# Kernel tuning notes

Measured on AMD Instinct MI355X. Metric: run time of the kernel, lower is better.

## Reference

```python
import jax, jax.numpy as jnp
import numpy as np
import math

DIM = 512
HEADS = 8
DH = DIM // HEADS
B, C, H, W = 2, 512, 48, 48


def setup_inputs() -> dict:
    key = jax.random.key(0)
    k1, k2, k3, k4 = jax.random.split(key, 4)
    x = jax.random.normal(k1, (B, C, H, W), dtype=jnp.float32)
    # torch Linear weights: [out_features, in_features]
    w_qkv = jax.random.normal(k2, (3 * DIM, DIM), dtype=jnp.float32) * (DIM ** -0.5)
    w_out = jax.random.normal(k3, (DIM, DIM), dtype=jnp.float32) * (DIM ** -0.5)
    b_out = jax.random.normal(k4, (DIM,), dtype=jnp.float32) * 0.01
    wavelength = jnp.asarray(0.1, dtype=jnp.float32)
    return {"x": x, "w_qkv": w_qkv, "w_out": w_out, "b_out": b_out, "wavelength": wavelength}


def reference(x, w_qkv, w_out, b_out, wavelength):
    b, c, h, w = x.shape
    n = h * w
    scale = DH ** -0.5

    x_flat = x.reshape(b, c, n).transpose(0, 2, 1)  # [B, N, C]
    qkv = jnp.einsum('bnc,dc->bnd', x_flat, w_qkv)   # [B, N, 3*DIM]
    q, k, v = jnp.split(qkv, 3, axis=-1)

    def to_heads(t):
        return t.reshape(b, n, HEADS, DH).transpose(0, 2, 1, 3)  # [B, h, N, dh]

    q, k, v = to_heads(q), to_heads(k), to_heads(v)

    dots = jnp.einsum('bhid,bhjd->bhij', q, k) * scale  # [B, h, N, N]

    # Fresnel interference bias over spatial positions
    yy, xx = jnp.meshgrid(jnp.arange(h), jnp.arange(w), indexing='ij')
    positions = jnp.stack([yy, xx], axis=-1).astype(jnp.float32).reshape(-1, 2)  # [N, 2]
    pos_diff = positions[None, :, :] - positions[:, None, :]  # [N, N, 2]
    distances = jnp.sqrt(jnp.sum(pos_diff ** 2, axis=-1) + 1e-8)  # [N, N]
    phase = 2.0 * math.pi * distances / (jnp.abs(wavelength) * h + 1e-6)
    interference = jnp.cos(phase)

    dots = dots + interference[None, None, :, :] * 0.1
    attn = jax.nn.softmax(dots, axis=-1)
    out = jnp.einsum('bhij,bhjd->bhid', attn, v)  # [B, h, N, dh]
    out = out.transpose(0, 2, 1, 3).reshape(b, n, HEADS * DH)  # [B, N, DIM]
    out = jnp.einsum('bnd,od->bno', out, w_out) + b_out
    return out.transpose(0, 2, 1).reshape(b, c, h, w)
```

## Files before the change

### kernel.cpp

```cpp
#include <hip/hip_runtime.h>
#include <math.h>

#define BB 2
#define CC 512
#define NN 2304
#define NH 8
#define DD 512
#define D3 1536
#define WIDTH 48
#define C1 0.18033688f

typedef _Float16 h8 __attribute__((ext_vector_type(8)));
typedef _Float16 h4 __attribute__((ext_vector_type(4)));
typedef _Float16 h2 __attribute__((ext_vector_type(2)));
typedef float f4 __attribute__((ext_vector_type(4)));

__device__ __forceinline__ void gload16(const void* g, void* s) {
  __builtin_amdgcn_global_load_lds(
      (const __attribute__((address_space(1))) unsigned int*)g,
      (__attribute__((address_space(3))) unsigned int*)s, 16, 0, 0);
}

__global__ __launch_bounds__(128) void btf_k(const float* __restrict__ wavp,
                                             _Float16* __restrict__ btf)
{
  const int t = threadIdx.x;
  const int qbk = blockIdx.x, ktk = blockIdx.y;
  const int w = t >> 6, quad = (t >> 4) & 3, l15 = t & 15;
  const float pc = 6.283185307179586f / (fabsf(wavp[0]) * (float)WIDTH + 1e-6f);
  _Float16* o = btf + (((size_t)qbk * 36 + ktk) * 128 + t) * 32;
#pragma unroll
  for (int g = 0; g < 4; ++g) {
    h8 v;
#pragma unroll
    for (int e = 0; e < 8; ++e) {
      const int j = g * 8 + e;
      const int nt = j >> 4, mt = (j >> 2) & 3, r = j & 3;
      const int q = qbk * 64 + w * 32 + nt * 16 + l15;
      const int k = ktk * 64 + mt * 16 + quad * 4 + r;
      const float dy = (float)(q / WIDTH) - (float)(k / WIDTH);
      const float dx = (float)(q % WIDTH) - (float)(k % WIDTH);
      const float dist = sqrtf(dy * dy + dx * dx + 1e-8f);
      v[e] = (_Float16)(0.1f * __cosf(dist * pc) * 1.44269504f);
    }
    *(h8*)(o + g * 8) = v;
  }
}

__global__ __launch_bounds__(256) void tx_k(const float* __restrict__ x,
                                            _Float16* __restrict__ xt)
{
  __shared__ float Ls[32][33];
  const int t = threadIdx.x;
  const int n0 = blockIdx.x * 32, c0 = blockIdx.y * 32, b = blockIdx.z;
#pragma unroll
  for (int p = 0; p < 4; ++p) {
    const int cl = (t >> 5) + p * 8, nl = t & 31;
    Ls[cl][nl] = x[((size_t)b * CC + c0 + cl) * NN + n0 + nl];
  }
  __syncthreads();
#pragma unroll
  for (int p = 0; p < 2; ++p) {
    const int nl = (t >> 4) + p * 16, cl = (t & 15) * 2;
    h2 v = {(_Float16)Ls[cl][nl], (_Float16)Ls[cl + 1][nl]};
    *(h2*)(xt + ((size_t)b * NN + n0 + nl) * CC + c0 + cl) = v;
  }
}

__global__ __launch_bounds__(256) void convw_k(const float* __restrict__ wq,
                                               const float* __restrict__ wo,
                                               _Float16* __restrict__ wqh,
                                               _Float16* __restrict__ woh)
{
  const int idx = blockIdx.x * 256 + threadIdx.x;
  const int NQ = (D3 * CC) / 4;
  if (idx < NQ) {
    float4 v = *(const float4*)(wq + (size_t)idx * 4);
    h4 o = {(_Float16)v.x, (_Float16)v.y, (_Float16)v.z, (_Float16)v.w};
    *(h4*)(wqh + (size_t)idx * 4) = o;
  } else {
    const int j = idx - NQ;
    float4 v = *(const float4*)(wo + (size_t)j * 4);
    h4 o = {(_Float16)v.x, (_Float16)v.y, (_Float16)v.z, (_Float16)v.w};
    *(h4*)(woh + (size_t)j * 4) = o;
  }
}

__global__ __launch_bounds__(256) void qkv_gemm_k(
    const _Float16* __restrict__ xt, const _Float16* __restrict__ wqh,
    _Float16* __restrict__ qb, _Float16* __restrict__ kb,
    _Float16* __restrict__ vb)
{
  __shared__ _Float16 Xs[128][32];
  __shared__ _Float16 Ws[128][32];
  const int t = threadIdx.x;
  const int lane = t & 63, w = t >> 6;
  const int l15 = lane & 15, quad = lane >> 4;
  const int wm = w & 1, wn = w >> 1;
  const int n0 = blockIdx.x * 128;
  const int d0 = blockIdx.y * 128;
  const int b  = blockIdx.z;
  const bool isv = (d0 >= 2 * DD);
  const _Float16* xb = xt + (size_t)b * NN * CC;

  const int srow = lane >> 2, scol = (lane & 3) * 8;

  f4 acc[4][4];
#pragma unroll
  for (int mt = 0; mt < 4; ++mt)
#pragma unroll
    for (int nt = 0; nt < 4; ++nt) acc[mt][nt] = (f4)(0.f);

  for (int c0 = 0; c0 < CC; c0 += 32) {
#pragma unroll
    for (int r = 0; r < 2; ++r) {
      const int ci = w + r * 4;
      const int row = ci * 16 + srow;
      gload16(xb + (size_t)(n0 + row) * CC + c0 + scol, &Xs[0][0] + ci * 512);
      gload16(wqh + (size_t)(d0 + row) * CC + c0 + scol, &Ws[0][0] + ci * 512);
    }
    __syncthreads();

    h8 wfr[4], xfr[4];
#pragma unroll
    for (int mt = 0; mt < 4; ++mt)
      wfr[mt] = *(const h8*)&Ws[wm * 64 + mt * 16 + l15][quad * 8];
#pragma unroll
    for (int nt = 0; nt < 4; ++nt)
      xfr[nt] = *(const h8*)&Xs[wn * 64 + nt * 16 + l15][quad * 8];

    if (!isv) {
#pragma unroll
      for (int mt = 0; mt < 4; ++mt)
#pragma unroll
        for (int nt = 0; nt < 4; ++nt)
          acc[mt][nt] = __builtin_amdgcn_mfma_f32_16x16x32_f16(
              wfr[mt], xfr[nt], acc[mt][nt], 0, 0, 0);
    } else {
#pragma unroll
      for (int mt = 0; mt < 4; ++mt)
#pragma unroll
        for (int nt = 0; nt < 4; ++nt)
          acc[mt][nt] = __builtin_amdgcn_mfma_f32_16x16x32_f16(
              xfr[nt], wfr[mt], acc[mt][nt], 0, 0, 0);
    }
    __syncthreads();
  }

  if (!isv) {
    const int which = d0 >> 9;
    _Float16* buf = which == 0 ? qb : kb;
    const int h = ((d0 & 511) >> 6) + wm;
#pragma unroll
    for (int mt = 0; mt < 4; ++mt) {
      const int dh = mt * 16 + quad * 4;
#pragma unroll
      for (int nt = 0; nt < 4; ++nt) {
        const int token = n0 + wn * 64 + nt * 16 + l15;
        h4 o = {(_Float16)acc[mt][nt][0], (_Float16)acc[mt][nt][1],
                (_Float16)acc[mt][nt][2], (_Float16)acc[mt][nt][3]};
        *(h4*)(buf + (((size_t)b * NH + h) * NN + token) * 64 + dh) = o;
      }
    }
  } else {
    const int h = ((d0 - 2 * DD) >> 6) + wm;
#pragma unroll
    for (int mt = 0; mt < 4; ++mt) {
      const int dh = mt * 16 + l15;
#pragma unroll
      for (int nt = 0; nt < 4; ++nt) {
        const int token = n0 + wn * 64 + nt * 16 + quad * 4;
        h4 o = {(_Float16)acc[mt][nt][0], (_Float16)acc[mt][nt][1],
                (_Float16)acc[mt][nt][2], (_Float16)acc[mt][nt][3]};
        *(h4*)(vb + (((size_t)b * NH + h) * 64 + dh) * NN + token) = o;
      }
    }
  }
}

__global__ __launch_bounds__(128, 3) void attn_k(
    const _Float16* __restrict__ qb, const _Float16* __restrict__ kb,
    const _Float16* __restrict__ vb, const _Float16* __restrict__ btf,
    _Float16* __restrict__ op, float* __restrict__ lp)
{
  __shared__ _Float16 Ks[64][72];
  __shared__ _Float16 Vs[64][72];
  __shared__ _Float16 Ps[64][72];

  const int t    = threadIdx.x;
  const int lane = t & 63;
  const int w    = t >> 6;
  const int l15  = lane & 15;
  const int quad = lane >> 4;
  const int qtile = blockIdx.x >> 1;
  const int khalf = blockIdx.x & 1;
  const int n0 = qtile * 64;
  const int h  = blockIdx.y;
  const int b  = blockIdx.z;
  const size_t base = ((size_t)b * NH + h) * NN * 64;
  const _Float16* qp = qb + base;
  const _Float16* kp = kb + base;
  const _Float16* vp = vb + base;

  h8 qf[2][2];
#pragma unroll
  for (int nt = 0; nt < 2; ++nt)
#pragma unroll
    for (int ks = 0; ks < 2; ++ks)
      qf[nt][ks] = *(const h8*)(qp + (size_t)(n0 + w * 32 + nt * 16 + l15) * 64 +
                                ks * 32 + quad * 8);

  f4 oc[4][2];
#pragma unroll
  for (int mt = 0; mt < 4; ++mt)
#pragma unroll
    for (int nt = 0; nt < 2; ++nt) oc[mt][nt] = (f4)(0.f);
  float lacc[2][4] = {};

  const _Float16* bp = btf + (((size_t)qtile * 36 + khalf * 18) * 128 + t) * 32;

  for (int kt = 0; kt < 18; ++kt) {
    const int k0 = (khalf * 18 + kt) * 64;
    h8 kr[4], vr[4], bfr[4];
#pragma unroll
    for (int r = 0; r < 4; ++r) {
      const int c = t + r * 128;
      const int row = c >> 3, off = (c & 7) * 8;
      kr[r] = *(const h8*)(kp + (size_t)(k0 + row) * 64 + off);
      vr[r] = *(const h8*)(vp + (size_t)row * NN + k0 + off);
      bfr[r] = *(const h8*)(bp + r * 8);
    }
    bp += 128 * 32;
    __syncthreads();
#pragma unroll
    for (int r = 0; r < 4; ++r) {
      const int c = t + r * 128;
      const int row = c >> 3, off = (c & 7) * 8;
      *(h8*)&Ks[row][off] = kr[r];
      *(h8*)&Vs[row][off] = vr[r];
    }
    __syncthreads();

    f4 st[4][2];
#pragma unroll
    for (int mt = 0; mt < 4; ++mt)
#pragma unroll
      for (int nt = 0; nt < 2; ++nt) st[mt][nt] = (f4)(0.f);
#pragma unroll
    for (int ks = 0; ks < 2; ++ks) {
#pragma unroll
      for (int mt = 0; mt < 4; ++mt) {
        h8 kf = *(const h8*)&Ks[mt * 16 + l15][ks * 32 + quad * 8];
#pragma unroll
        for (int nt = 0; nt < 2; ++nt)
          st[mt][nt] = __builtin_amdgcn_mfma_f32_16x16x32_f16(
              kf, qf[nt][ks], st[mt][nt], 0, 0, 0);
      }
    }

#pragma unroll
    for (int nt = 0; nt < 2; ++nt) {
      const int q = w * 32 + nt * 16 + l15;
#pragma unroll
      for (int mt = 0; mt < 4; ++mt) {
        h4 pk;
#pragma unroll
        for (int r = 0; r < 4; ++r) {
          const int j = nt * 16 + mt * 4 + r;
          const float bias = (float)bfr[j >> 3][j & 7];
          const float p = __builtin_exp2f(st[mt][nt][r] * C1 + bias);
          lacc[nt][r] += p;
          pk[r] = (_Float16)p;
        }
        *(h4*)&Ps[q][mt * 16 + quad * 4] = pk;
      }
    }

#pragma unroll
    for (int ks = 0; ks < 2; ++ks) {
      h8 pf[2];
#pragma unroll
      for (int nt = 0; nt < 2; ++nt)
        pf[nt] = *(const h8*)&Ps[w * 32 + nt * 16 + l15][ks * 32 + quad * 8];
#pragma unroll
      for (int mt = 0; mt < 4; ++mt) {
        h8 vf = *(const h8*)&Vs[mt * 16 + l15][ks * 32 + quad * 8];
#pragma unroll
        for (int nt = 0; nt < 2; ++nt)
          oc[mt][nt] = __builtin_amdgcn_mfma_f32_16x16x32_f16(
              vf, pf[nt], oc[mt][nt], 0, 0, 0);
      }
    }
  }

#pragma unroll
  for (int nt = 0; nt < 2; ++nt) {
    float l = lacc[nt][0] + lacc[nt][1] + lacc[nt][2] + lacc[nt][3];
    l += __shfl_xor(l, 16);
    l += __shfl_xor(l, 32);
    const float inv = 1.f / l;
    const int qi = n0 + w * 32 + nt * 16 + l15;
    _Float16* od = op + (size_t)khalf * BB * NN * DD +
                   ((size_t)b * NN + qi) * DD + h * 64;
#pragma unroll
    for (int mt = 0; mt < 4; ++mt) {
      const int dh = mt * 16 + quad * 4;
      h4 o = {(_Float16)(oc[mt][nt][0] * inv), (_Float16)(oc[mt][nt][1] * inv),
              (_Float16)(oc[mt][nt][2] * inv), (_Float16)(oc[mt][nt][3] * inv)};
      *(h4*)(od + dh) = o;
    }
    if (quad == 0)
      lp[(size_t)khalf * BB * NH * NN + ((size_t)b * NH + h) * NN + qi] = l;
  }
}

__global__ __launch_bounds__(256) void comb_k(
    const _Float16* __restrict__ op, const float* __restrict__ lp,
    _Float16* __restrict__ ho)
{
  const int idx = blockIdx.x * 256 + threadIdx.x;
  const int d8 = idx & 63;
  const int bn = idx >> 6;
  const int n = bn % NN, b = bn / NN;
  const int h = d8 >> 3;
  const float l0 = lp[((size_t)b * NH + h) * NN + n];
  const float l1 = lp[(size_t)BB * NH * NN + ((size_t)b * NH + h) * NN + n];
  const float inv = 1.f / (l0 + l1);
  const float w0 = l0 * inv, w1 = l1 * inv;
  h8 o0 = *(const h8*)(op + (size_t)bn * DD + d8 * 8);
  h8 o1 = *(const h8*)(op + (size_t)BB * NN * DD + (size_t)bn * DD + d8 * 8);
  h8 r;
#pragma unroll
  for (int i = 0; i < 8; ++i)
    r[i] = (_Float16)((float)o0[i] * w0 + (float)o1[i] * w1);
  *(h8*)(ho + (size_t)bn * DD + d8 * 8) = r;
}

__global__ __launch_bounds__(64) void out_gemm_k(
    const _Float16* __restrict__ ho, const _Float16* __restrict__ woh,
    const float* __restrict__ bias, float* __restrict__ out)
{
  __shared__ _Float16 Hs[64][32];
  __shared__ _Float16 Ws2[64][32];
  const int t = threadIdx.x;
  const int l15 = t & 15, quad = t >> 4;
  const int n0 = blockIdx.x * 64;
  const int o0 = blockIdx.y * 64;
  const int b  = blockIdx.z;
  const int srow = t >> 2, scol = (t & 3) * 8;

  f4 acc[4][4];
#pragma unroll
  for (int mt = 0; mt < 4; ++mt)
#pragma unroll
    for (int nt = 0; nt < 4; ++nt) acc[mt][nt] = (f4)(0.f);

  for (int c0 = 0; c0 < DD; c0 += 32) {
#pragma unroll
    for (int ci = 0; ci < 4; ++ci) {
      const int row = ci * 16 + srow;
      gload16(ho + ((size_t)b * NN + n0 + row) * DD + c0 + scol,
              &Hs[0][0] + ci * 512);
      gload16(woh + (size_t)(o0 + row) * DD + c0 + scol,
              &Ws2[0][0] + ci * 512);
    }
    __syncthreads();
    h8 hf[4], wf[4];
#pragma unroll
    for (int mt = 0; mt < 4; ++mt)
      hf[mt] = *(const h8*)&Hs[mt * 16 + l15][quad * 8];
#pragma unroll
    for (int nt = 0; nt < 4; ++nt)
      wf[nt] = *(const h8*)&Ws2[nt * 16 + l15][quad * 8];
#pragma unroll
    for (int mt = 0; mt < 4; ++mt)
#pragma unroll
      for (int nt = 0; nt < 4; ++nt)
        acc[mt][nt] = __builtin_amdgcn_mfma_f32_16x16x32_f16(
            hf[mt], wf[nt], acc[mt][nt], 0, 0, 0);
    __syncthreads();
  }

#pragma unroll
  for (int nt = 0; nt < 4; ++nt) {
    const int o = o0 + nt * 16 + l15;
    const float bv = bias[o];
#pragma unroll
    for (int mt = 0; mt < 4; ++mt) {
      const int token = n0 + mt * 16 + quad * 4;
      float4 v = {acc[mt][nt][0] + bv, acc[mt][nt][1] + bv,
                  acc[mt][nt][2] + bv, acc[mt][nt][3] + bv};
      *(float4*)(out + ((size_t)b * DD + o) * NN + token) = v;
    }
  }
}

extern "C" void kernel_launch(void* const* d_in, const int* in_sizes, int n_in,
                              void* d_out, int out_size, void* d_ws, size_t ws_size,
                              hipStream_t stream)
{
  (void)in_sizes; (void)n_in; (void)out_size; (void)ws_size;
  const float* x     = (const float*)d_in[0];
  const float* w_qkv = (const float*)d_in[1];
  const float* w_out = (const float*)d_in[2];
  const float* b_out = (const float*)d_in[3];
  const float* wav   = (const float*)d_in[4];
  float* out = (float*)d_out;

  const size_t SZ  = (size_t)BB * NH * NN * 64;
  const size_t BTF = (size_t)36 * 36 * 128 * 32;

  _Float16* qb  = (_Float16*)d_ws;
  _Float16* kb  = qb + SZ;
  _Float16* vb  = kb + SZ;
  _Float16* btf = vb + SZ;
  _Float16* op  = btf + BTF;
  float*    lpf = (float*)(op + 2 * SZ);
  _Float16* woh = (_Float16*)(lpf + 2 * (size_t)BB * NH * NN);
  _Float16* ho  = btf;
  _Float16* xt  = op;
  _Float16* wqh = op + SZ;

  btf_k     <<<dim3(36, 36), 128, 0, stream>>>(wav, btf);
  tx_k      <<<dim3(NN / 32, CC / 32, BB), 256, 0, stream>>>(x, xt);
  convw_k   <<<dim3((D3 * CC + DD * DD) / 1024), 256, 0, stream>>>(w_qkv, w_out, wqh, woh);
  qkv_gemm_k<<<dim3(NN / 128, D3 / 128, BB), 256, 0, stream>>>(xt, wqh, qb, kb, vb);
  attn_k    <<<dim3(NN / 64 * 2, NH, BB), 128, 0, stream>>>(qb, kb, vb, btf, op, lpf);
  comb_k    <<<dim3((BB * NN * 64) / 256), 256, 0, stream>>>(op, lpf, ho);
  out_gemm_k<<<dim3(NN / 64, DD / 64, BB), 64, 0, stream>>>(ho, woh, b_out, out);
}
```

Measured before the change: 168.4 us.

## Compress bias table by tile-difference symmetry, split K three ways, fuse prep kernels

The three preprocessing kernels (bias table, transpose of x, weight conversion) are merged into one launch. The 36x36 bias tile table is shrunk to 213 tiles, indexed by query-key tile offset and query tile mod 3. This works because 64-token tiles shift the 48-wide grid by a periodic pattern. The attention kernel now splits keys three ways instead of two and reuses the K shared-memory buffer for P, which drops the Ps array and raises occupancy to 4 blocks. Packed fp16 conversion is used for P. The combine step merges three partials, which adds an extra sync per tile and more partial-output traffic.

```diff
diff --git a/kernel.cpp b/kernel.cpp
--- a/kernel.cpp
+++ b/kernel.cpp
@@ -10,6 +10,10 @@
 #define WIDTH 48
 #define C1 0.18033688f
 
+#define KSPLIT 3
+#define KTILES 12
+#define NTBL 213
+
 typedef _Float16 h8 __attribute__((ext_vector_type(8)));
 typedef _Float16 h4 __attribute__((ext_vector_type(4)));
 typedef _Float16 h2 __attribute__((ext_vector_type(2)));
@@ -21,68 +25,72 @@
       (__attribute__((address_space(3))) unsigned int*)s, 16, 0, 0);
 }
 
-__global__ __launch_bounds__(128) void btf_k(const float* __restrict__ wavp,
-                                             _Float16* __restrict__ btf)
-{
-  const int t = threadIdx.x;
-  const int qbk = blockIdx.x, ktk = blockIdx.y;
-  const int w = t >> 6, quad = (t >> 4) & 3, l15 = t & 15;
-  const float pc = 6.283185307179586f / (fabsf(wavp[0]) * (float)WIDTH + 1e-6f);
-  _Float16* o = btf + (((size_t)qbk * 36 + ktk) * 128 + t) * 32;
-#pragma unroll
-  for (int g = 0; g < 4; ++g) {
-    h8 v;
-#pragma unroll
-    for (int e = 0; e < 8; ++e) {
-      const int j = g * 8 + e;
-      const int nt = j >> 4, mt = (j >> 2) & 3, r = j & 3;
-      const int q = qbk * 64 + w * 32 + nt * 16 + l15;
-      const int k = ktk * 64 + mt * 16 + quad * 4 + r;
-      const float dy = (float)(q / WIDTH) - (float)(k / WIDTH);
-      const float dx = (float)(q % WIDTH) - (float)(k % WIDTH);
-      const float dist = sqrtf(dy * dy + dx * dx + 1e-8f);
-      v[e] = (_Float16)(0.1f * __cosf(dist * pc) * 1.44269504f);
-    }
-    *(h8*)(o + g * 8) = v;
-  }
-}
-
-__global__ __launch_bounds__(256) void tx_k(const float* __restrict__ x,
-                                            _Float16* __restrict__ xt)
+__global__ __launch_bounds__(256) void prep_k(
+    const float* __restrict__ x, const float* __restrict__ wq,
+    const float* __restrict__ wo, const float* __restrict__ wavp,
+    _Float16* __restrict__ xt, _Float16* __restrict__ wqh,
+    _Float16* __restrict__ woh, _Float16* __restrict__ btf)
 {
   __shared__ float Ls[32][33];
   const int t = threadIdx.x;
-  const int n0 = blockIdx.x * 32, c0 = blockIdx.y * 32, b = blockIdx.z;
-#pragma unroll
-  for (int p = 0; p < 4; ++p) {
-    const int cl = (t >> 5) + p * 8, nl = t & 31;
-    Ls[cl][nl] = x[((size_t)b * CC + c0 + cl) * NN + n0 + nl];
-  }
-  __syncthreads();
-#pragma unroll
-  for (int p = 0; p < 2; ++p) {
-    const int nl = (t >> 4) + p * 16, cl = (t & 15) * 2;
-    h2 v = {(_Float16)Ls[cl][nl], (_Float16)Ls[cl + 1][nl]};
-    *(h2*)(xt + ((size_t)b * NN + n0 + nl) * CC + c0 + cl) = v;
-  }
-}
-
-__global__ __launch_bounds__(256) void convw_k(const float* __restrict__ wq,
-                                               const float* __restrict__ wo,
-                                               _Float16* __restrict__ wqh,
-                                               _Float16* __restrict__ woh)
-{
-  const int idx = blockIdx.x * 256 + threadIdx.x;
-  const int NQ = (D3 * CC) / 4;
-  if (idx < NQ) {
-    float4 v = *(const float4*)(wq + (size_t)idx * 4);
-    h4 o = {(_Float16)v.x, (_Float16)v.y, (_Float16)v.z, (_Float16)v.w};
-    *(h4*)(wqh + (size_t)idx * 4) = o;
+  const int e = blockIdx.x;
+
+  if (e < 2304) {
+    const int n0 = (e % 72) * 32;
+    const int c0 = ((e / 72) % 16) * 32;
+    const int b  = e / 1152;
+#pragma unroll
+    for (int p = 0; p < 4; ++p) {
+      const int cl = (t >> 5) + p * 8, nl = t & 31;
+      Ls[cl][nl] = x[((size_t)b * CC + c0 + cl) * NN + n0 + nl];
+    }
+    __syncthreads();
+#pragma unroll
+    for (int p = 0; p < 2; ++p) {
+      const int nl = (t >> 4) + p * 16, cl = (t & 15) * 2;
+      h2 v = {(_Float16)Ls[cl][nl], (_Float16)Ls[cl + 1][nl]};
+      *(h2*)(xt + ((size_t)b * NN + n0 + nl) * CC + c0 + cl) = v;
+    }
+  } else if (e < 3328) {
+    const int idx = (e - 2304) * 256 + t;
+    const int NQ = (D3 * CC) / 4;
+    if (idx < NQ) {
+      float4 v = *(const float4*)(wq + (size_t)idx * 4);
+      h4 o = {(_Float16)v.x, (_Float16)v.y, (_Float16)v.z, (_Float16)v.w};
+      *(h4*)(wqh + (size_t)idx * 4) = o;
+    } else {
+      const int j = idx - NQ;
+      float4 v = *(const float4*)(wo + (size_t)j * 4);
+      h4 o = {(_Float16)v.x, (_Float16)v.y, (_Float16)v.z, (_Float16)v.w};
+      *(h4*)(woh + (size_t)j * 4) = o;
+    }
   } else {
-    const int j = idx - NQ;
-    float4 v = *(const float4*)(wo + (size_t)j * 4);
-    h4 o = {(_Float16)v.x, (_Float16)v.y, (_Float16)v.z, (_Float16)v.w};
-    *(h4*)(woh + (size_t)j * 4) = o;
+    const int tbl = (e - 3328) * 2 + (t >> 7);
+    if (tbl < NTBL) {
+      const int tid = t & 127;
+      const int dD = tbl / 3, qm = tbl % 3;
+      const int qt0 = qm + 36;
+      const int kt0 = qt0 - (dD - 35);
+      const int w = tid >> 6, quad = (tid >> 4) & 3, l15 = tid & 15;
+      const float pc = 6.283185307179586f / (fabsf(wavp[0]) * (float)WIDTH + 1e-6f);
+      _Float16* o = btf + ((size_t)tbl * 128 + tid) * 32;
+#pragma unroll
+      for (int g = 0; g < 4; ++g) {
+        h8 v;
+#pragma unroll
+        for (int el = 0; el < 8; ++el) {
+          const int j = g * 8 + el;
+          const int nt = j >> 4, mt = (j >> 2) & 3, r = j & 3;
+          const int q = qt0 * 64 + w * 32 + nt * 16 + l15;
+          const int k = kt0 * 64 + mt * 16 + quad * 4 + r;
+          const float dy = (float)(q / WIDTH) - (float)(k / WIDTH);
+          const float dx = (float)(q % WIDTH) - (float)(k % WIDTH);
+          const float dist = sqrtf(dy * dy + dx * dx + 1e-8f);
+          v[el] = (_Float16)(0.1f * __cosf(dist * pc) * 1.44269504f);
+        }
+        *(h8*)(o + g * 8) = v;
+      }
+    }
   }
 }
 
@@ -178,22 +186,21 @@
   }
 }
 
-__global__ __launch_bounds__(128, 3) void attn_k(
+__global__ __launch_bounds__(128, 4) void attn_k(
     const _Float16* __restrict__ qb, const _Float16* __restrict__ kb,
     const _Float16* __restrict__ vb, const _Float16* __restrict__ btf,
     _Float16* __restrict__ op, float* __restrict__ lp)
 {
   __shared__ _Float16 Ks[64][72];
   __shared__ _Float16 Vs[64][72];
-  __shared__ _Float16 Ps[64][72];
 
   const int t    = threadIdx.x;
   const int lane = t & 63;
   const int w    = t >> 6;
   const int l15  = lane & 15;
   const int quad = lane >> 4;
-  const int qtile = blockIdx.x >> 1;
-  const int khalf = blockIdx.x & 1;
+  const int qtile = blockIdx.x / KSPLIT;
+  const int kq    = blockIdx.x % KSPLIT;
   const int n0 = qtile * 64;
   const int h  = blockIdx.y;
   const int b  = blockIdx.z;
@@ -215,12 +222,14 @@
   for (int mt = 0; mt < 4; ++mt)
 #pragma unroll
     for (int nt = 0; nt < 2; ++nt) oc[mt][nt] = (f4)(0.f);
-  float lacc[2][4] = {};
-
-  const _Float16* bp = btf + (((size_t)qtile * 36 + khalf * 18) * 128 + t) * 32;
-
-  for (int kt = 0; kt < 18; ++kt) {
-    const int k0 = (khalf * 18 + kt) * 64;
+  float lac[2][2] = {};
+
+  const int ktg0 = kq * KTILES;
+  const _Float16* bp =
+      btf + ((size_t)((qtile - ktg0 + 35) * 3 + qtile % 3) * 128 + t) * 32;
+
+  for (int kt = 0; kt < KTILES; ++kt) {
+    const int k0 = (ktg0 + kt) * 64;
     h8 kr[4], vr[4], bfr[4];
 #pragma unroll
     for (int r = 0; r < 4; ++r) {
@@ -230,7 +239,7 @@
       vr[r] = *(const h8*)(vp + (size_t)row * NN + k0 + off);
       bfr[r] = *(const h8*)(bp + r * 8);
     }
-    bp += 128 * 32;
+    bp -= 3 * 128 * 32;
     __syncthreads();
 #pragma unroll
     for (int r = 0; r < 4; ++r) {
@@ -258,21 +267,29 @@
       }
     }
 
+    __syncthreads();
+
 #pragma unroll
     for (int nt = 0; nt < 2; ++nt) {
       const int q = w * 32 + nt * 16 + l15;
 #pragma unroll
       for (int mt = 0; mt < 4; ++mt) {
-        h4 pk;
-#pragma unroll
-        for (int r = 0; r < 4; ++r) {
-          const int j = nt * 16 + mt * 4 + r;
-          const float bias = (float)bfr[j >> 3][j & 7];
-          const float p = __builtin_exp2f(st[mt][nt][r] * C1 + bias);
-          lacc[nt][r] += p;
-          pk[r] = (_Float16)p;
-        }
-        *(h4*)&Ps[q][mt * 16 + quad * 4] = pk;
+        const int jb = nt * 16 + mt * 4;
+        const float b0 = (float)bfr[jb >> 3][(jb & 7) + 0];
+        const float b1 = (float)bfr[jb >> 3][(jb & 7) + 1];
+        const float b2 = (float)bfr[jb >> 3][(jb & 7) + 2];
+        const float b3 = (float)bfr[jb >> 3][(jb & 7) + 3];
+        const float p0 = __builtin_exp2f(st[mt][nt][0] * C1 + b0);
+        const float p1 = __builtin_exp2f(st[mt][nt][1] * C1 + b1);
+        const float p2 = __builtin_exp2f(st[mt][nt][2] * C1 + b2);
+        const float p3 = __builtin_exp2f(st[mt][nt][3] * C1 + b3);
+        lac[nt][0] += p0 + p1;
+        lac[nt][1] += p2 + p3;
+        const auto plo = __builtin_amdgcn_cvt_pkrtz(p0, p1);
+        const auto phi = __builtin_amdgcn_cvt_pkrtz(p2, p3);
+        h4 pk = {(_Float16)plo[0], (_Float16)plo[1],
+                 (_Float16)phi[0], (_Float16)phi[1]};
+        *(h4*)&Ks[q][mt * 16 + quad * 4] = pk;
       }
     }
 
@@ -281,7 +298,7 @@
       h8 pf[2];
 #pragma unroll
       for (int nt = 0; nt < 2; ++nt)
-        pf[nt] = *(const h8*)&Ps[w * 32 + nt * 16 + l15][ks * 32 + quad * 8];
+        pf[nt] = *(const h8*)&Ks[w * 32 + nt * 16 + l15][ks * 32 + quad * 8];
 #pragma unroll
       for (int mt = 0; mt < 4; ++mt) {
         h8 vf = *(const h8*)&Vs[mt * 16 + l15][ks * 32 + quad * 8];
@@ -295,12 +312,12 @@
 
 #pragma unroll
   for (int nt = 0; nt < 2; ++nt) {
-    float l = lacc[nt][0] + lacc[nt][1] + lacc[nt][2] + lacc[nt][3];
+    float l = lac[nt][0] + lac[nt][1];
     l += __shfl_xor(l, 16);
     l += __shfl_xor(l, 32);
     const float inv = 1.f / l;
     const int qi = n0 + w * 32 + nt * 16 + l15;
-    _Float16* od = op + (size_t)khalf * BB * NN * DD +
+    _Float16* od = op + (size_t)kq * BB * NN * DD +
                    ((size_t)b * NN + qi) * DD + h * 64;
 #pragma unroll
     for (int mt = 0; mt < 4; ++mt) {
@@ -310,7 +327,7 @@
       *(h4*)(od + dh) = o;
     }
     if (quad == 0)
-      lp[(size_t)khalf * BB * NH * NN + ((size_t)b * NH + h) * NN + qi] = l;
+      lp[(size_t)kq * BB * NH * NN + ((size_t)b * NH + h) * NN + qi] = l;
   }
 }
 
@@ -323,16 +340,21 @@
   const int bn = idx >> 6;
   const int n = bn % NN, b = bn / NN;
   const int h = d8 >> 3;
-  const float l0 = lp[((size_t)b * NH + h) * NN + n];
-  const float l1 = lp[(size_t)BB * NH * NN + ((size_t)b * NH + h) * NN + n];
-  const float inv = 1.f / (l0 + l1);
-  const float w0 = l0 * inv, w1 = l1 * inv;
+  const size_t SL = (size_t)BB * NH * NN;
+  const size_t SO = (size_t)BB * NN * DD;
+  const size_t li = ((size_t)b * NH + h) * NN + n;
+  const float l0 = lp[li];
+  const float l1 = lp[SL + li];
+  const float l2 = lp[2 * SL + li];
+  const float inv = 1.f / (l0 + l1 + l2);
+  const float w0 = l0 * inv, w1 = l1 * inv, w2 = l2 * inv;
   h8 o0 = *(const h8*)(op + (size_t)bn * DD + d8 * 8);
-  h8 o1 = *(const h8*)(op + (size_t)BB * NN * DD + (size_t)bn * DD + d8 * 8);
+  h8 o1 = *(const h8*)(op + SO + (size_t)bn * DD + d8 * 8);
+  h8 o2 = *(const h8*)(op + 2 * SO + (size_t)bn * DD + d8 * 8);
   h8 r;
 #pragma unroll
   for (int i = 0; i < 8; ++i)
-    r[i] = (_Float16)((float)o0[i] * w0 + (float)o1[i] * w1);
+    r[i] = (_Float16)((float)o0[i] * w0 + (float)o1[i] * w1 + (float)o2[i] * w2);
   *(h8*)(ho + (size_t)bn * DD + d8 * 8) = r;
 }
 
@@ -408,24 +430,23 @@
   float* out = (float*)d_out;
 
   const size_t SZ  = (size_t)BB * NH * NN * 64;
-  const size_t BTF = (size_t)36 * 36 * 128 * 32;
+  const size_t BTF = (size_t)NTBL * 128 * 32;
 
   _Float16* qb  = (_Float16*)d_ws;
   _Float16* kb  = qb + SZ;
   _Float16* vb  = kb + SZ;
   _Float16* btf = vb + SZ;
   _Float16* op  = btf + BTF;
-  float*    lpf = (float*)(op + 2 * SZ);
-  _Float16* woh = (_Float16*)(lpf + 2 * (size_t)BB * NH * NN);
-  _Float16* ho  = btf;
+  float*    lpf = (float*)(op + 3 * SZ);
+  _Float16* woh = (_Float16*)(lpf + 3 * (size_t)BB * NH * NN);
+  _Float16* ho  = qb;
   _Float16* xt  = op;
   _Float16* wqh = op + SZ;
 
-  btf_k     <<<dim3(36, 36), 128, 0, stream>>>(wav, btf);
-  tx_k      <<<dim3(NN / 32, CC / 32, BB), 256, 0, stream>>>(x, xt);
-  convw_k   <<<dim3((D3 * CC + DD * DD) / 1024), 256, 0, stream>>>(w_qkv, w_out, wqh, woh);
+  prep_k    <<<dim3(2304 + 1024 + 107), 256, 0, stream>>>(x, w_qkv, w_out, wav,
+                                                          xt, wqh, woh, btf);
   qkv_gemm_k<<<dim3(NN / 128, D3 / 128, BB), 256, 0, stream>>>(xt, wqh, qb, kb, vb);
-  attn_k    <<<dim3(NN / 64 * 2, NH, BB), 128, 0, stream>>>(qb, kb, vb, btf, op, lpf);
+  attn_k    <<<dim3(NN / 64 * KSPLIT, NH, BB), 128, 0, stream>>>(qb, kb, vb, btf, op, lpf);
   comb_k    <<<dim3((BB * NN * 64) / 256), 256, 0, stream>>>(op, lpf, ho);
   out_gemm_k<<<dim3(NN / 64, DD / 64, BB), 64, 0, stream>>>(ho, woh, b_out, out);
 }
```

After: 173.5 us. 3.0% more time.
